# Kernel tuning notes

Measured on AMD Instinct MI355X. Metric: run time of the kernel, lower is better.

The kernel has to match this reference:

```python
import jax, jax.numpy as jnp
import numpy as np

D = 512
M_FUT = 3
EPS = 1e-12


def _lin(x, W, b):
    return x @ W + b


def _svd_orthogonalize(m):
    # m: [B, 9] -> [B, 3, 3] SO(3) via SVD orthogonalization (special Procrustes)
    m = m.reshape(-1, 3, 3)
    norm = jnp.maximum(jnp.linalg.norm(m, axis=-1, keepdims=True), EPS)
    mt = jnp.swapaxes(m / norm, -1, -2)          # normalize rows, then transpose
    u, s, vh = jnp.linalg.svd(mt, full_matrices=False)
    v = jnp.swapaxes(vh, -1, -2)                 # torch.svd returns V, jax returns V^H
    ut = jnp.swapaxes(u, -1, -2)
    det = jnp.linalg.det(jnp.matmul(v, ut))      # [B]
    v_adj = jnp.concatenate([v[:, :, :-1], v[:, :, -1:] * det[:, None, None]], axis=2)
    return jnp.matmul(v_adj, ut)


def setup_inputs() -> dict:
    key = jax.random.key(0)
    ks = iter(jax.random.split(key, 40))
    B, N, M = 32, 3, M_FUT
    ph = pw = 37
    BN, hw = B * N, ph * pw
    sc = 1.0 / np.sqrt(D)
    rn = lambda *shape: (jax.random.normal(next(ks), shape, dtype=jnp.float32) * sc)
    inp = {
        'feat': jax.random.normal(next(ks), (BN, hw, D), dtype=jnp.float32),
        'patch_h': ph, 'patch_w': pw, 'batch_size': B, 'num_current_frames': N,
        # two ResConvBlocks, three 512x512 Linears each (in==out -> skip is identity)
        'W_res': rn(2, 3, D, D), 'b_res': rn(2, 3, D),
        # TemporalCameraMLP
        'W_cur1': rn(D, D), 'b_cur1': rn(D), 'W_cur2': rn(D, D), 'b_cur2': rn(D),
        'W_tp1': rn(D, D), 'b_tp1': rn(D), 'W_tp2': rn(D, D * M), 'b_tp2': rn(D * M),
        'W_fut1': rn(D, D), 'b_fut1': rn(D), 'W_fut2': rn(D, D), 'b_fut2': rn(D),
        # more_mlps
        'W_m1': rn(D, D), 'b_m1': rn(D), 'W_m2': rn(D, D), 'b_m2': rn(D),
        # pose heads (fp32)
        'W_t': rn(D, 3), 'b_t': rn(3), 'W_r': rn(D, 9), 'b_r': rn(9),
    }
    return inp


def reference(feat, patch_h, patch_w, batch_size, num_current_frames,
              W_res, b_res, W_cur1, b_cur1, W_cur2, b_cur2,
              W_tp1, b_tp1, W_tp2, b_tp2, W_fut1, b_fut1, W_fut2, b_fut2,
              W_m1, b_m1, W_m2, b_m2, W_t, b_t, W_r, b_r):
    B, N = batch_size, num_current_frames
    M = W_tp2.shape[1] // W_tp2.shape[0]
    # stacked residual 1x1-conv (Linear) blocks
    for i in range(2):
        x = jax.nn.relu(_lin(feat, W_res[i, 0], b_res[i, 0]))
        x = jax.nn.relu(_lin(x, W_res[i, 1], b_res[i, 1]))
        x = jax.nn.relu(_lin(x, W_res[i, 2], b_res[i, 2]))
        feat = feat + x
    # AdaptiveAvgPool2d(1) over patch grid == mean over hw
    pooled = feat.mean(axis=1)                                  # [BN, D]
    # TemporalCameraMLP
    cur = _lin(jax.nn.relu(_lin(pooled, W_cur1, b_cur1)), W_cur2, b_cur2)   # [BN, D]
    gctx = pooled.reshape(B, N, -1).mean(axis=1)                            # [B, D]
    tf = _lin(jax.nn.relu(_lin(gctx, W_tp1, b_tp1)), W_tp2, b_tp2)          # [B, D*M]
    tf = tf.reshape(B * M, -1)
    fut = _lin(jax.nn.relu(_lin(tf, W_fut1, b_fut1)), W_fut2, b_fut2)       # [B*M, D]
    allf = jnp.concatenate([cur, fut], axis=0)                              # [B*(N+M), D]
    h = jax.nn.relu(_lin(jax.nn.relu(_lin(allf, W_m1, b_m1)), W_m2, b_m2))
    # pose head in fp32
    hf = h.astype(jnp.float32)
    out_t = _lin(hf, W_t, b_t)                                  # [newBN, 3]
    out_r = _lin(hf, W_r, b_r)                                  # [newBN, 9]
    r = _svd_orthogonalize(out_r)                               # [newBN, 3, 3]
    newBN = allf.shape[0]
    pose = jnp.zeros((newBN, 4, 4), dtype=jnp.float32)
    pose = pose.at[:, :3, :3].set(r)
    pose = pose.at[:, :3, 3].set(out_t)
    pose = pose.at[:, 3, 3].set(1.0)
    return pose
```

## Files before the change

### kernel.cpp

```cpp
#include <hip/hip_runtime.h>


typedef unsigned short u16;
typedef __attribute__((ext_vector_type(8))) short short8;
typedef __attribute__((ext_vector_type(16))) float f32x16;

constexpr int  DDIM   = 512;
constexpr long R_ROWS = 96L * 1369L;
constexpr long R_PAD  = 2054L * 64L;

__device__ __forceinline__ u16 f2b(float f) {
  union { float f; unsigned u; } x; x.f = f;
  unsigned r = (x.u + 0x7FFFu + ((x.u >> 16) & 1u)) >> 16;
  return (u16)r;
}
__device__ __forceinline__ float b2f(u16 b) {
  union { unsigned u; float f; } x; x.u = ((unsigned)b) << 16;
  return x.f;
}

__global__ void convert_feat_k(const float* __restrict__ in, u16* __restrict__ out) {
  long i4 = ((long)blockIdx.x * 256 + threadIdx.x) * 4;
  if (i4 >= R_PAD * DDIM) return;
  ushort4 o;
  if (i4 < R_ROWS * DDIM) {
    float4 v = *(const float4*)(in + i4);
    o.x = f2b(v.x); o.y = f2b(v.y); o.z = f2b(v.z); o.w = f2b(v.w);
  } else {
    o.x = 0; o.y = 0; o.z = 0; o.w = 0;
  }
  *(ushort4*)(out + i4) = o;
}

__global__ void pack_w_k(const float* __restrict__ W, u16* __restrict__ Wp) {
  int tid = blockIdx.x * 256 + threadIdx.x;
  if (tid >= 6 * 262144) return;
  int g  = tid >> 18, t2 = tid & 262143;
  int ks = t2 >> 13, t3 = t2 & 8191;
  int q  = t3 >> 12, t4 = t3 & 4095;
  int n  = t4 >> 3,  j  = t4 & 7;
  int k  = ks * 16 + q * 8 + j;
  Wp[tid] = f2b(W[(long)g * 262144 + (long)k * 512 + n]);
}

__global__ __launch_bounds__(256, 2)
void fused_res_k(u16* __restrict__ Xg, const u16* __restrict__ Wp,
                 const float* __restrict__ bres) {
  __shared__ u16 Yb[64 * 512];
  const int tid = threadIdx.x;
  const int lane = tid & 63;
  const int wvC  = tid >> 6;
  const int l31  = lane & 31;
  const int q    = lane >> 5;
  const long rowBase = (long)blockIdx.x * 64;

#pragma unroll
  for (int i = 0; i < 16; ++i) {
    int L = i * 256 + tid;
    int r = L >> 6, cS = L & 63;
    int c = cS ^ r;
    const u16* ga = Xg + (rowBase + r) * DDIM + c * 8;
    __builtin_amdgcn_global_load_lds(
        (const __attribute__((address_space(1))) void*)ga,
        (__attribute__((address_space(3))) void*)&Yb[L * 8], 16, 0, 0);
  }
  __syncthreads();

  for (int l = 0; l < 3; ++l) {
    const u16* wl = Wp + (long)l * 262144;
    const float* bias = bres + l * 512;

    f32x16 acc[4][2];
#pragma unroll
    for (int mi = 0; mi < 4; ++mi)
#pragma unroll
      for (int nb = 0; nb < 2; ++nb)
#pragma unroll
        for (int e = 0; e < 16; ++e) acc[mi][nb][e] = 0.f;

#pragma unroll 4
    for (int ks = 0; ks < 32; ++ks) {
      const int k8 = ks * 2 + q;
      const u16* wk = wl + ((long)(k8) * 512 + wvC * 128 + l31) * 8;
      short8 wf[4];
#pragma unroll
      for (int mi = 0; mi < 4; ++mi)
        wf[mi] = *(const short8*)(wk + mi * 32 * 8);
      short8 xf[2];
#pragma unroll
      for (int nb = 0; nb < 2; ++nb) {
        int r = nb * 32 + l31;
        xf[nb] = *(const short8*)&Yb[(r * 64 + (k8 ^ r)) * 8];
      }
#pragma unroll
      for (int mi = 0; mi < 4; ++mi)
#pragma unroll
        for (int nb = 0; nb < 2; ++nb)
          acc[mi][nb] = __builtin_amdgcn_mfma_f32_32x32x16_bf16(
              wf[mi], xf[nb], acc[mi][nb], 0, 0, 0);
    }
    __syncthreads();

    if (l < 2) {
#pragma unroll
      for (int mi = 0; mi < 4; ++mi) {
#pragma unroll
        for (int j2 = 0; j2 < 4; ++j2) {
          int n0 = wvC * 128 + mi * 32 + 4 * q + 8 * j2;
          float4 bv = *(const float4*)(bias + n0);
#pragma unroll
          for (int nb = 0; nb < 2; ++nb) {
            int r = nb * 32 + l31;
            ushort4 pk;
            pk.x = f2b(fmaxf(acc[mi][nb][4 * j2 + 0] + bv.x, 0.f));
            pk.y = f2b(fmaxf(acc[mi][nb][4 * j2 + 1] + bv.y, 0.f));
            pk.z = f2b(fmaxf(acc[mi][nb][4 * j2 + 2] + bv.z, 0.f));
            pk.w = f2b(fmaxf(acc[mi][nb][4 * j2 + 3] + bv.w, 0.f));
            *(ushort4*)&Yb[(r * 64 + ((n0 >> 3) ^ r)) * 8 + (n0 & 7)] = pk;
          }
        }
      }
      __syncthreads();
    } else {
#pragma unroll
      for (int mi = 0; mi < 4; ++mi) {
#pragma unroll
        for (int j2 = 0; j2 < 4; ++j2) {
          int n0 = wvC * 128 + mi * 32 + 4 * q + 8 * j2;
          float4 bv = *(const float4*)(bias + n0);
#pragma unroll
          for (int nb = 0; nb < 2; ++nb) {
            int r = nb * 32 + l31;
            u16* gp = Xg + (rowBase + r) * DDIM + n0;
            ushort4 xv = *(const ushort4*)gp;
            ushort4 pk;
            pk.x = f2b(fmaxf(acc[mi][nb][4 * j2 + 0] + bv.x, 0.f) + b2f(xv.x));
            pk.y = f2b(fmaxf(acc[mi][nb][4 * j2 + 1] + bv.y, 0.f) + b2f(xv.y));
            pk.z = f2b(fmaxf(acc[mi][nb][4 * j2 + 2] + bv.z, 0.f) + b2f(xv.z));
            pk.w = f2b(fmaxf(acc[mi][nb][4 * j2 + 3] + bv.w, 0.f) + b2f(xv.w));
            *(ushort4*)gp = pk;
          }
        }
      }
    }
  }
}

__global__ void zero_k(float* p, int n) {
  int i = blockIdx.x * 256 + threadIdx.x;
  if (i < n) p[i] = 0.f;
}

__global__ void pool_k(const u16* __restrict__ feat, float* __restrict__ pooled) {
  int bn = blockIdx.x, ch = blockIdx.y, d = threadIdx.x;
  int p0 = ch * 172, p1 = p0 + 172;
  if (p1 > 1369) p1 = 1369;
  float s = 0.f;
  long base = ((long)bn * 1369 + p0) * DDIM + d;
  for (int p = p0; p < p1; ++p) { s += b2f(feat[base]); base += DDIM; }
  atomicAdd(&pooled[bn * DDIM + d], s * (1.0f / 1369.0f));
}

__global__ void gctx_k(const float* __restrict__ pooled, float* __restrict__ gctx) {
  int i = blockIdx.x * 256 + threadIdx.x;
  if (i >= 32 * DDIM) return;
  int b = i >> 9, d = i & 511;
  const float* p = pooled + (long)b * 3 * DDIM + d;
  gctx[i] = (p[0] + p[DDIM] + p[2 * DDIM]) * (1.0f / 3.0f);
}

template <bool RELU>
__global__ void lin_k(const float* __restrict__ in, const float* __restrict__ W,
                      const float* __restrict__ bias, float* __restrict__ out,
                      int K, int N) {
  int n = blockIdx.x * 256 + threadIdx.x;
  int r = blockIdx.y;
  if (n >= N) return;
  float acc = bias[n];
  const float* xi = in + (long)r * K;
#pragma unroll 8
  for (int k = 0; k < K; ++k) acc = fmaf(xi[k], W[(long)k * N + n], acc);
  if (RELU) acc = fmaxf(acc, 0.f);
  out[(long)r * N + n] = acc;
}

__global__ void pose_k(const float* __restrict__ h,
                       const float* __restrict__ Wt, const float* __restrict__ bt,
                       const float* __restrict__ Wr, const float* __restrict__ br,
                       float* __restrict__ out) {
  int row = blockIdx.x;
  int lane = threadIdx.x;
  const float* hr = h + (long)row * DDIM;
  float part[12];
#pragma unroll
  for (int c = 0; c < 12; ++c) {
    float acc = 0.f;
    for (int k = lane; k < DDIM; k += 64) {
      float wvv = (c < 3) ? Wt[k * 3 + c] : Wr[k * 9 + (c - 3)];
      acc += hr[k] * wvv;
    }
#pragma unroll
    for (int off = 32; off > 0; off >>= 1) acc += __shfl_down(acc, off);
    part[c] = acc;
  }
  if (lane != 0) return;

  double t3[3];
  for (int i = 0; i < 3; ++i) t3[i] = (double)part[i] + (double)bt[i];
  double m[3][3];
  for (int i = 0; i < 3; ++i)
    for (int j = 0; j < 3; ++j) m[i][j] = (double)part[3 + i * 3 + j] + (double)br[i * 3 + j];
  for (int i = 0; i < 3; ++i) {
    double nn = sqrt(m[i][0] * m[i][0] + m[i][1] * m[i][1] + m[i][2] * m[i][2]);
    if (nn < 1e-12) nn = 1e-12;
    m[i][0] /= nn; m[i][1] /= nn; m[i][2] /= nn;
  }
  double Km[3][3];
  for (int a = 0; a < 3; ++a)
    for (int b = 0; b < 3; ++b) {
      double s = 0;
      for (int i = 0; i < 3; ++i) s += m[i][a] * m[i][b];
      Km[a][b] = s;
    }
  double V[3][3] = {{1, 0, 0}, {0, 1, 0}, {0, 0, 1}};
  const int PQ[3][2] = {{0, 1}, {0, 2}, {1, 2}};
  for (int sweep = 0; sweep < 20; ++sweep) {
    for (int e = 0; e < 3; ++e) {
      int p = PQ[e][0], qq = PQ[e][1];
      double apq = Km[p][qq];
      if (apq == 0.0) continue;
      double tau = (Km[qq][qq] - Km[p][p]) / (2.0 * apq);
      double tt = (tau >= 0.0 ? 1.0 : -1.0) / (fabs(tau) + sqrt(1.0 + tau * tau));
      double cc = 1.0 / sqrt(1.0 + tt * tt), ss = tt * cc;
      for (int k = 0; k < 3; ++k) { double a1 = Km[p][k], a2 = Km[qq][k]; Km[p][k] = cc * a1 - ss * a2; Km[qq][k] = ss * a1 + cc * a2; }
      for (int k = 0; k < 3; ++k) { double a1 = Km[k][p], a2 = Km[k][qq]; Km[k][p] = cc * a1 - ss * a2; Km[k][qq] = ss * a1 + cc * a2; }
      for (int k = 0; k < 3; ++k) { double a1 = V[k][p], a2 = V[k][qq]; V[k][p] = cc * a1 - ss * a2; V[k][qq] = ss * a1 + cc * a2; }
    }
  }
  double lam[3] = {Km[0][0], Km[1][1], Km[2][2]};
  int o0 = 0, o1 = 1, o2 = 2; double detV = 1.0;
  if (lam[o0] < lam[o1]) { int t = o0; o0 = o1; o1 = t; detV = -detV; }
  if (lam[o1] < lam[o2]) { int t = o1; o1 = o2; o2 = t; detV = -detV; }
  if (lam[o0] < lam[o1]) { int t = o0; o0 = o1; o1 = t; detV = -detV; }
  double v0[3] = {V[0][o0], V[1][o0], V[2][o0]};
  double v1[3] = {V[0][o1], V[1][o1], V[2][o1]};
  double v2[3] = {V[0][o2], V[1][o2], V[2][o2]};
  double u0[3], u1[3];
  for (int i = 0; i < 3; ++i) u0[i] = m[i][0] * v0[0] + m[i][1] * v0[1] + m[i][2] * v0[2];
  double n0 = sqrt(u0[0] * u0[0] + u0[1] * u0[1] + u0[2] * u0[2]); if (n0 < 1e-30) n0 = 1e-30;
  for (int i = 0; i < 3; ++i) u0[i] /= n0;
  for (int i = 0; i < 3; ++i) u1[i] = m[i][0] * v1[0] + m[i][1] * v1[1] + m[i][2] * v1[2];
  double d01 = u0[0] * u1[0] + u0[1] * u1[1] + u0[2] * u1[2];
  for (int i = 0; i < 3; ++i) u1[i] -= d01 * u0[i];
  double n1 = sqrt(u1[0] * u1[0] + u1[1] * u1[1] + u1[2] * u1[2]); if (n1 < 1e-30) n1 = 1e-30;
  for (int i = 0; i < 3; ++i) u1[i] /= n1;
  double u2[3] = {u0[1] * u1[2] - u0[2] * u1[1],
                  u0[2] * u1[0] - u0[0] * u1[2],
                  u0[0] * u1[1] - u0[1] * u1[0]};
  float* o = out + (long)row * 16;
  for (int i = 0; i < 3; ++i) {
    for (int j = 0; j < 3; ++j)
      o[i * 4 + j] = (float)(u0[i] * v0[j] + u1[i] * v1[j] + detV * u2[i] * v2[j]);
    o[i * 4 + 3] = (float)t3[i];
  }
  o[12] = 0.f; o[13] = 0.f; o[14] = 0.f; o[15] = 1.f;
}

extern "C" void kernel_launch(void* const* d_in, const int* in_sizes, int n_in,
                              void* d_out, int out_size, void* d_ws, size_t ws_size,
                              hipStream_t stream) {
  (void)in_sizes; (void)n_in; (void)out_size; (void)ws_size;
  const float* feat   = (const float*)d_in[0];
  const float* W_res  = (const float*)d_in[5];
  const float* b_res  = (const float*)d_in[6];
  const float* W_cur1 = (const float*)d_in[7];
  const float* b_cur1 = (const float*)d_in[8];
  const float* W_cur2 = (const float*)d_in[9];
  const float* b_cur2 = (const float*)d_in[10];
  const float* W_tp1  = (const float*)d_in[11];
  const float* b_tp1  = (const float*)d_in[12];
  const float* W_tp2  = (const float*)d_in[13];
  const float* b_tp2  = (const float*)d_in[14];
  const float* W_fut1 = (const float*)d_in[15];
  const float* b_fut1 = (const float*)d_in[16];
  const float* W_fut2 = (const float*)d_in[17];
  const float* b_fut2 = (const float*)d_in[18];
  const float* W_m1   = (const float*)d_in[19];
  const float* b_m1   = (const float*)d_in[20];
  const float* W_m2   = (const float*)d_in[21];
  const float* b_m2   = (const float*)d_in[22];
  const float* W_t    = (const float*)d_in[23];
  const float* b_t    = (const float*)d_in[24];
  const float* W_r    = (const float*)d_in[25];
  const float* b_r    = (const float*)d_in[26];

  char* ws = (char*)d_ws;
  const size_t SZ_BIG = (size_t)R_PAD * DDIM * 2;
  u16* A  = (u16*)(ws);
  u16* Wp = (u16*)(ws + SZ_BIG);
  char* tail = ws + SZ_BIG + (size_t)6 * 262144 * 2;
  float* pooled = (float*)(tail);
  float* gctx   = pooled + 96 * 512;
  float* tmp    = gctx + 32 * 512;
  float* tfb    = tmp + 192 * 512;
  float* allf   = tfb + 32 * 1536;
  float* h2     = allf + 192 * 512;
  float* outp   = (float*)d_out;

  convert_feat_k<<<65728, 256, 0, stream>>>(feat, A);
  pack_w_k<<<6144, 256, 0, stream>>>(W_res, Wp);

  fused_res_k<<<2054, 256, 0, stream>>>(A, Wp,                 b_res);
  fused_res_k<<<2054, 256, 0, stream>>>(A, Wp + 3L * 262144,   b_res + 3 * 512);

  zero_k<<<(96 * 512 + 255) / 256, 256, 0, stream>>>(pooled, 96 * 512);
  pool_k<<<dim3(96, 8), 512, 0, stream>>>(A, pooled);
  gctx_k<<<(32 * 512 + 255) / 256, 256, 0, stream>>>(pooled, gctx);

  lin_k<true ><<<dim3(2, 96),  256, 0, stream>>>(pooled, W_cur1, b_cur1, tmp, 512, 512);
  lin_k<false><<<dim3(2, 96),  256, 0, stream>>>(tmp, W_cur2, b_cur2, allf, 512, 512);
  lin_k<true ><<<dim3(2, 32),  256, 0, stream>>>(gctx, W_tp1, b_tp1, tmp, 512, 512);
  lin_k<false><<<dim3(6, 32),  256, 0, stream>>>(tmp, W_tp2, b_tp2, tfb, 512, 1536);
  lin_k<true ><<<dim3(2, 96),  256, 0, stream>>>(tfb, W_fut1, b_fut1, tmp, 512, 512);
  lin_k<false><<<dim3(2, 96),  256, 0, stream>>>(tmp, W_fut2, b_fut2, allf + 96 * 512, 512, 512);
  lin_k<true ><<<dim3(2, 192), 256, 0, stream>>>(allf, W_m1, b_m1, tmp, 512, 512);
  lin_k<true ><<<dim3(2, 192), 256, 0, stream>>>(tmp, W_m2, b_m2, h2, 512, 512);

  pose_k<<<192, 64, 0, stream>>>(h2, W_t, b_t, W_r, b_r, outp);
}
```

Baseline: 1.675 ms.

## Fuse feat conversion and both residual blocks into one trunk kernel, fuse MLP tail

Folds the fp32-to-bf16 conversion into a single trunk kernel that runs all six 512x512 layers of both residual blocks with activations kept in LDS. It uses 512 threads with 64 columns per wave and software-pipelined weight and LDS fragment loads. The nine small MLP and pose launches become one 24-block tail kernel that chains the layers through shared memory. This removes several global round-trips of the large activation tensor and many launch overheads, at the cost of a low-parallelism tail kernel and a different register/occupancy profile in the trunk.

```diff
diff --git a/kernel.cpp b/kernel.cpp
--- a/kernel.cpp
+++ b/kernel.cpp
@@ -19,129 +19,125 @@
   return x.f;
 }
 
-__global__ void convert_feat_k(const float* __restrict__ in, u16* __restrict__ out) {
-  long i4 = ((long)blockIdx.x * 256 + threadIdx.x) * 4;
-  if (i4 >= R_PAD * DDIM) return;
-  ushort4 o;
-  if (i4 < R_ROWS * DDIM) {
-    float4 v = *(const float4*)(in + i4);
-    o.x = f2b(v.x); o.y = f2b(v.y); o.z = f2b(v.z); o.w = f2b(v.w);
-  } else {
-    o.x = 0; o.y = 0; o.z = 0; o.w = 0;
-  }
-  *(ushort4*)(out + i4) = o;
-}
-
 __global__ void pack_w_k(const float* __restrict__ W, u16* __restrict__ Wp) {
   int tid = blockIdx.x * 256 + threadIdx.x;
   if (tid >= 6 * 262144) return;
   int g  = tid >> 18, t2 = tid & 262143;
-  int ks = t2 >> 13, t3 = t2 & 8191;
-  int q  = t3 >> 12, t4 = t3 & 4095;
-  int n  = t4 >> 3,  j  = t4 & 7;
-  int k  = ks * 16 + q * 8 + j;
+  int k8 = t2 >> 12, t3 = t2 & 4095;
+  int n  = t3 >> 3,  j  = t3 & 7;
+  int k  = k8 * 8 + j;
   Wp[tid] = f2b(W[(long)g * 262144 + (long)k * 512 + n]);
 }
 
-__global__ __launch_bounds__(256, 2)
-void fused_res_k(u16* __restrict__ Xg, const u16* __restrict__ Wp,
-                 const float* __restrict__ bres) {
+__global__ __launch_bounds__(512, 3)
+void trunk_k(const float* __restrict__ feat, u16* __restrict__ A,
+             const u16* __restrict__ Wp, const float* __restrict__ bres) {
   __shared__ u16 Yb[64 * 512];
-  const int tid = threadIdx.x;
+  const int tid  = threadIdx.x;
   const int lane = tid & 63;
-  const int wvC  = tid >> 6;
+  const int wv   = tid >> 6;
   const int l31  = lane & 31;
   const int q    = lane >> 5;
+  const int colBase = wv * 64;
   const long rowBase = (long)blockIdx.x * 64;
 
 #pragma unroll
   for (int i = 0; i < 16; ++i) {
-    int L = i * 256 + tid;
-    int r = L >> 6, cS = L & 63;
-    int c = cS ^ r;
-    const u16* ga = Xg + (rowBase + r) * DDIM + c * 8;
-    __builtin_amdgcn_global_load_lds(
-        (const __attribute__((address_space(1))) void*)ga,
-        (__attribute__((address_space(3))) void*)&Yb[L * 8], 16, 0, 0);
+    int f4 = i * 512 + tid;
+    int r = f4 >> 7, c4 = f4 & 127;
+    int k = c4 * 4;
+    long grow = rowBase + r;
+    float4 v = {0.f, 0.f, 0.f, 0.f};
+    if (grow < R_ROWS) v = *(const float4*)(feat + grow * DDIM + k);
+    ushort4 pk;
+    pk.x = f2b(v.x); pk.y = f2b(v.y); pk.z = f2b(v.z); pk.w = f2b(v.w);
+    int k8 = c4 >> 1, half = c4 & 1;
+    *(ushort4*)&Yb[(r * 64 + (k8 ^ r)) * 8 + half * 4] = pk;
+    *(ushort4*)(A + grow * DDIM + k) = pk;
   }
   __syncthreads();
 
-  for (int l = 0; l < 3; ++l) {
+  for (int l = 0; l < 6; ++l) {
     const u16* wl = Wp + (long)l * 262144;
     const float* bias = bres + l * 512;
 
-    f32x16 acc[4][2];
-#pragma unroll
-    for (int mi = 0; mi < 4; ++mi)
+    f32x16 acc[2][2];
+#pragma unroll
+    for (int mi = 0; mi < 2; ++mi)
 #pragma unroll
       for (int nb = 0; nb < 2; ++nb)
 #pragma unroll
         for (int e = 0; e < 16; ++e) acc[mi][nb][e] = 0.f;
 
-#pragma unroll 4
-    for (int ks = 0; ks < 32; ++ks) {
-      const int k8 = ks * 2 + q;
-      const u16* wk = wl + ((long)(k8) * 512 + wvC * 128 + l31) * 8;
-      short8 wf[4];
-#pragma unroll
-      for (int mi = 0; mi < 4; ++mi)
-        wf[mi] = *(const short8*)(wk + mi * 32 * 8);
-      short8 xf[2];
+    auto loadW = [&](short8* w, int ks) {
+      const u16* wk = wl + ((long)(ks * 2 + q) * 512 + colBase + l31) * 8;
+      w[0] = *(const short8*)wk;
+      w[1] = *(const short8*)(wk + 32 * 8);
+    };
+    auto loadX = [&](short8* x, int ks) {
+      int k8 = ks * 2 + q;
 #pragma unroll
       for (int nb = 0; nb < 2; ++nb) {
         int r = nb * 32 + l31;
-        xf[nb] = *(const short8*)&Yb[(r * 64 + (k8 ^ r)) * 8];
+        x[nb] = *(const short8*)&Yb[(r * 64 + (k8 ^ r)) * 8];
       }
-#pragma unroll
-      for (int mi = 0; mi < 4; ++mi)
+    };
+
+    short8 wA[2], wB[2], xA[2];
+    loadW(wA, 0); loadW(wB, 1); loadX(xA, 0);
+#pragma unroll
+    for (int ks = 0; ks < 32; ++ks) {
+      short8 wC[2], xN[2];
+      loadW(wC, ks < 30 ? ks + 2 : ks);
+      loadX(xN, ks < 31 ? ks + 1 : ks);
+#pragma unroll
+      for (int mi = 0; mi < 2; ++mi)
 #pragma unroll
         for (int nb = 0; nb < 2; ++nb)
           acc[mi][nb] = __builtin_amdgcn_mfma_f32_32x32x16_bf16(
-              wf[mi], xf[nb], acc[mi][nb], 0, 0, 0);
+              wA[mi], xA[nb], acc[mi][nb], 0, 0, 0);
+      wA[0] = wB[0]; wA[1] = wB[1];
+      wB[0] = wC[0]; wB[1] = wC[1];
+      xA[0] = xN[0]; xA[1] = xN[1];
     }
     __syncthreads();
 
-    if (l < 2) {
-#pragma unroll
-      for (int mi = 0; mi < 4; ++mi) {
-#pragma unroll
-        for (int j2 = 0; j2 < 4; ++j2) {
-          int n0 = wvC * 128 + mi * 32 + 4 * q + 8 * j2;
-          float4 bv = *(const float4*)(bias + n0);
-#pragma unroll
-          for (int nb = 0; nb < 2; ++nb) {
-            int r = nb * 32 + l31;
-            ushort4 pk;
-            pk.x = f2b(fmaxf(acc[mi][nb][4 * j2 + 0] + bv.x, 0.f));
-            pk.y = f2b(fmaxf(acc[mi][nb][4 * j2 + 1] + bv.y, 0.f));
-            pk.z = f2b(fmaxf(acc[mi][nb][4 * j2 + 2] + bv.z, 0.f));
-            pk.w = f2b(fmaxf(acc[mi][nb][4 * j2 + 3] + bv.w, 0.f));
-            *(ushort4*)&Yb[(r * 64 + ((n0 >> 3) ^ r)) * 8 + (n0 & 7)] = pk;
-          }
+#pragma unroll
+    for (int mi = 0; mi < 2; ++mi) {
+#pragma unroll
+      for (int j2 = 0; j2 < 4; ++j2) {
+        int n0 = colBase + mi * 32 + 4 * q + 8 * j2;
+        float4 bv = *(const float4*)(bias + n0);
+#pragma unroll
+        for (int nb = 0; nb < 2; ++nb) {
+          int r = nb * 32 + l31;
+          ushort4 pk;
+          pk.x = f2b(fmaxf(acc[mi][nb][4 * j2 + 0] + bv.x, 0.f));
+          pk.y = f2b(fmaxf(acc[mi][nb][4 * j2 + 1] + bv.y, 0.f));
+          pk.z = f2b(fmaxf(acc[mi][nb][4 * j2 + 2] + bv.z, 0.f));
+          pk.w = f2b(fmaxf(acc[mi][nb][4 * j2 + 3] + bv.w, 0.f));
+          *(ushort4*)&Yb[(r * 64 + ((n0 >> 3) ^ r)) * 8 + (n0 & 7)] = pk;
         }
       }
+    }
+    __syncthreads();
+
+    if (l == 2 || l == 5) {
+#pragma unroll
+      for (int i = 0; i < 8; ++i) {
+        int L = i * 512 + tid;
+        int r = L >> 6, cS = L & 63, c = cS ^ r;
+        long off = (rowBase + r) * DDIM + c * 8;
+        short8 y = *(const short8*)&Yb[L * 8];
+        short8 rs = *(const short8*)(A + off);
+        short8 o;
+#pragma unroll
+        for (int e = 0; e < 8; ++e)
+          o[e] = (short)f2b(b2f((u16)y[e]) + b2f((u16)rs[e]));
+        *(short8*)(A + off) = o;
+        if (l == 2) *(short8*)&Yb[L * 8] = o;
+      }
       __syncthreads();
-    } else {
-#pragma unroll
-      for (int mi = 0; mi < 4; ++mi) {
-#pragma unroll
-        for (int j2 = 0; j2 < 4; ++j2) {
-          int n0 = wvC * 128 + mi * 32 + 4 * q + 8 * j2;
-          float4 bv = *(const float4*)(bias + n0);
-#pragma unroll
-          for (int nb = 0; nb < 2; ++nb) {
-            int r = nb * 32 + l31;
-            u16* gp = Xg + (rowBase + r) * DDIM + n0;
-            ushort4 xv = *(const ushort4*)gp;
-            ushort4 pk;
-            pk.x = f2b(fmaxf(acc[mi][nb][4 * j2 + 0] + bv.x, 0.f) + b2f(xv.x));
-            pk.y = f2b(fmaxf(acc[mi][nb][4 * j2 + 1] + bv.y, 0.f) + b2f(xv.y));
-            pk.z = f2b(fmaxf(acc[mi][nb][4 * j2 + 2] + bv.z, 0.f) + b2f(xv.z));
-            pk.w = f2b(fmaxf(acc[mi][nb][4 * j2 + 3] + bv.w, 0.f) + b2f(xv.w));
-            *(ushort4*)gp = pk;
-          }
-        }
-      }
     }
   }
 }
@@ -151,65 +147,22 @@
   if (i < n) p[i] = 0.f;
 }
 
-__global__ void pool_k(const u16* __restrict__ feat, float* __restrict__ pooled) {
+__global__ void pool_k(const u16* __restrict__ A, float* __restrict__ pooled) {
   int bn = blockIdx.x, ch = blockIdx.y, d = threadIdx.x;
   int p0 = ch * 172, p1 = p0 + 172;
   if (p1 > 1369) p1 = 1369;
   float s = 0.f;
   long base = ((long)bn * 1369 + p0) * DDIM + d;
-  for (int p = p0; p < p1; ++p) { s += b2f(feat[base]); base += DDIM; }
+#pragma unroll 4
+  for (int p = p0; p < p1; ++p) { s += b2f(A[base]); base += DDIM; }
   atomicAdd(&pooled[bn * DDIM + d], s * (1.0f / 1369.0f));
 }
 
-__global__ void gctx_k(const float* __restrict__ pooled, float* __restrict__ gctx) {
-  int i = blockIdx.x * 256 + threadIdx.x;
-  if (i >= 32 * DDIM) return;
-  int b = i >> 9, d = i & 511;
-  const float* p = pooled + (long)b * 3 * DDIM + d;
-  gctx[i] = (p[0] + p[DDIM] + p[2 * DDIM]) * (1.0f / 3.0f);
-}
-
-template <bool RELU>
-__global__ void lin_k(const float* __restrict__ in, const float* __restrict__ W,
-                      const float* __restrict__ bias, float* __restrict__ out,
-                      int K, int N) {
-  int n = blockIdx.x * 256 + threadIdx.x;
-  int r = blockIdx.y;
-  if (n >= N) return;
-  float acc = bias[n];
-  const float* xi = in + (long)r * K;
-#pragma unroll 8
-  for (int k = 0; k < K; ++k) acc = fmaf(xi[k], W[(long)k * N + n], acc);
-  if (RELU) acc = fmaxf(acc, 0.f);
-  out[(long)r * N + n] = acc;
-}
-
-__global__ void pose_k(const float* __restrict__ h,
-                       const float* __restrict__ Wt, const float* __restrict__ bt,
-                       const float* __restrict__ Wr, const float* __restrict__ br,
-                       float* __restrict__ out) {
-  int row = blockIdx.x;
-  int lane = threadIdx.x;
-  const float* hr = h + (long)row * DDIM;
-  float part[12];
-#pragma unroll
-  for (int c = 0; c < 12; ++c) {
-    float acc = 0.f;
-    for (int k = lane; k < DDIM; k += 64) {
-      float wvv = (c < 3) ? Wt[k * 3 + c] : Wr[k * 9 + (c - 3)];
-      acc += hr[k] * wvv;
-    }
-#pragma unroll
-    for (int off = 32; off > 0; off >>= 1) acc += __shfl_down(acc, off);
-    part[c] = acc;
-  }
-  if (lane != 0) return;
-
-  double t3[3];
-  for (int i = 0; i < 3; ++i) t3[i] = (double)part[i] + (double)bt[i];
+__device__ void svd_pose(const float* pin, float* o) {
+  double t3[3] = {pin[0], pin[1], pin[2]};
   double m[3][3];
   for (int i = 0; i < 3; ++i)
-    for (int j = 0; j < 3; ++j) m[i][j] = (double)part[3 + i * 3 + j] + (double)br[i * 3 + j];
+    for (int j = 0; j < 3; ++j) m[i][j] = (double)pin[3 + i * 3 + j];
   for (int i = 0; i < 3; ++i) {
     double nn = sqrt(m[i][0] * m[i][0] + m[i][1] * m[i][1] + m[i][2] * m[i][2]);
     if (nn < 1e-12) nn = 1e-12;
@@ -257,13 +210,96 @@
   double u2[3] = {u0[1] * u1[2] - u0[2] * u1[1],
                   u0[2] * u1[0] - u0[0] * u1[2],
                   u0[0] * u1[1] - u0[1] * u1[0]};
-  float* o = out + (long)row * 16;
   for (int i = 0; i < 3; ++i) {
     for (int j = 0; j < 3; ++j)
       o[i * 4 + j] = (float)(u0[i] * v0[j] + u1[i] * v1[j] + detV * u2[i] * v2[j]);
     o[i * 4 + 3] = (float)t3[i];
   }
   o[12] = 0.f; o[13] = 0.f; o[14] = 0.f; o[15] = 1.f;
+}
+
+__global__ void tail_k(const float* __restrict__ pooled,
+                       const float* Wc1, const float* bc1, const float* Wc2, const float* bc2,
+                       const float* Wt1, const float* bt1, const float* Wt2, const float* bt2,
+                       const float* Wf1, const float* bf1, const float* Wf2, const float* bf2,
+                       const float* Wm1, const float* bm1, const float* Wm2, const float* bm2,
+                       const float* Wt, const float* bt, const float* Wr, const float* br,
+                       float* __restrict__ out) {
+  __shared__ float bufA[8][512];
+  __shared__ float bufB[8][512];
+  __shared__ float pose_in[8][12];
+  const int blk = blockIdx.x;
+  const int tid = threadIdx.x;
+  const bool isFut = blk >= 12;
+  int m0 = 0, b0 = 0;
+  if (!isFut) {
+    int r0 = blk * 8;
+#pragma unroll
+    for (int r = 0; r < 8; ++r) bufA[r][tid] = pooled[(r0 + r) * 512 + tid];
+  } else {
+    int f = blk - 12; m0 = f >> 2; b0 = (f & 3) * 8;
+#pragma unroll
+    for (int r = 0; r < 8; ++r) {
+      int b = b0 + r;
+      bufA[r][tid] = (pooled[(b * 3 + 0) * 512 + tid] +
+                      pooled[(b * 3 + 1) * 512 + tid] +
+                      pooled[(b * 3 + 2) * 512 + tid]) * (1.0f / 3.0f);
+    }
+  }
+  __syncthreads();
+
+  auto layer = [&](float (*in)[512], float (*ob)[512], const float* W, int ldw,
+                   int coff, const float* b, bool relu) {
+    int n = tid;
+    float acc[8];
+#pragma unroll
+    for (int r = 0; r < 8; ++r) acc[r] = b[coff + n];
+    for (int k = 0; k < 512; k += 4) {
+      float w0 = W[(long)(k + 0) * ldw + coff + n];
+      float w1 = W[(long)(k + 1) * ldw + coff + n];
+      float w2 = W[(long)(k + 2) * ldw + coff + n];
+      float w3 = W[(long)(k + 3) * ldw + coff + n];
+#pragma unroll
+      for (int r = 0; r < 8; ++r) {
+        float4 x = *(const float4*)&in[r][k];
+        acc[r] = fmaf(x.x, w0, acc[r]);
+        acc[r] = fmaf(x.y, w1, acc[r]);
+        acc[r] = fmaf(x.z, w2, acc[r]);
+        acc[r] = fmaf(x.w, w3, acc[r]);
+      }
+    }
+#pragma unroll
+    for (int r = 0; r < 8; ++r) ob[r][n] = relu ? fmaxf(acc[r], 0.f) : acc[r];
+    __syncthreads();
+  };
+
+  if (!isFut) {
+    layer(bufA, bufB, Wc1, 512, 0, bc1, true);
+    layer(bufB, bufA, Wc2, 512, 0, bc2, false);
+    layer(bufA, bufB, Wm1, 512, 0, bm1, true);
+    layer(bufB, bufA, Wm2, 512, 0, bm2, true);
+  } else {
+    layer(bufA, bufB, Wt1, 512, 0, bt1, true);
+    layer(bufB, bufA, Wt2, 1536, m0 * 512, bt2, false);
+    layer(bufA, bufB, Wf1, 512, 0, bf1, true);
+    layer(bufB, bufA, Wf2, 512, 0, bf2, false);
+    layer(bufA, bufB, Wm1, 512, 0, bm1, true);
+    layer(bufB, bufA, Wm2, 512, 0, bm2, true);
+  }
+  int r = tid >> 6, c = tid & 63;
+  if (c < 12) {
+    float acc = (c < 3) ? bt[c] : br[c - 3];
+    for (int k = 0; k < 512; ++k) {
+      float w = (c < 3) ? Wt[k * 3 + c] : Wr[k * 9 + (c - 3)];
+      acc = fmaf(bufA[r][k], w, acc);
+    }
+    pose_in[r][c] = acc;
+  }
+  __syncthreads();
+  if (tid < 8) {
+    int grow = isFut ? (96 + (b0 + tid) * 3 + m0) : (blk * 8 + tid);
+    svd_pose(&pose_in[tid][0], out + (long)grow * 16);
+  }
 }
 
 extern "C" void kernel_launch(void* const* d_in, const int* in_sizes, int n_in,
@@ -298,33 +334,17 @@
   const size_t SZ_BIG = (size_t)R_PAD * DDIM * 2;
   u16* A  = (u16*)(ws);
   u16* Wp = (u16*)(ws + SZ_BIG);
-  char* tail = ws + SZ_BIG + (size_t)6 * 262144 * 2;
-  float* pooled = (float*)(tail);
-  float* gctx   = pooled + 96 * 512;
-  float* tmp    = gctx + 32 * 512;
-  float* tfb    = tmp + 192 * 512;
-  float* allf   = tfb + 32 * 1536;
-  float* h2     = allf + 192 * 512;
+  float* pooled = (float*)(ws + SZ_BIG + (size_t)6 * 262144 * 2);
   float* outp   = (float*)d_out;
 
-  convert_feat_k<<<65728, 256, 0, stream>>>(feat, A);
   pack_w_k<<<6144, 256, 0, stream>>>(W_res, Wp);
-
-  fused_res_k<<<2054, 256, 0, stream>>>(A, Wp,                 b_res);
-  fused_res_k<<<2054, 256, 0, stream>>>(A, Wp + 3L * 262144,   b_res + 3 * 512);
+  trunk_k<<<2054, 512, 0, stream>>>(feat, A, Wp, b_res);
 
   zero_k<<<(96 * 512 + 255) / 256, 256, 0, stream>>>(pooled, 96 * 512);
   pool_k<<<dim3(96, 8), 512, 0, stream>>>(A, pooled);
-  gctx_k<<<(32 * 512 + 255) / 256, 256, 0, stream>>>(pooled, gctx);
-
-  lin_k<true ><<<dim3(2, 96),  256, 0, stream>>>(pooled, W_cur1, b_cur1, tmp, 512, 512);
-  lin_k<false><<<dim3(2, 96),  256, 0, stream>>>(tmp, W_cur2, b_cur2, allf, 512, 512);
-  lin_k<true ><<<dim3(2, 32),  256, 0, stream>>>(gctx, W_tp1, b_tp1, tmp, 512, 512);
-  lin_k<false><<<dim3(6, 32),  256, 0, stream>>>(tmp, W_tp2, b_tp2, tfb, 512, 1536);
-  lin_k<true ><<<dim3(2, 96),  256, 0, stream>>>(tfb, W_fut1, b_fut1, tmp, 512, 512);
-  lin_k<false><<<dim3(2, 96),  256, 0, stream>>>(tmp, W_fut2, b_fut2, allf + 96 * 512, 512, 512);
-  lin_k<true ><<<dim3(2, 192), 256, 0, stream>>>(allf, W_m1, b_m1, tmp, 512, 512);
-  lin_k<true ><<<dim3(2, 192), 256, 0, stream>>>(tmp, W_m2, b_m2, h2, 512, 512);
-
-  pose_k<<<192, 64, 0, stream>>>(h2, W_t, b_t, W_r, b_r, outp);
-}
+
+  tail_k<<<24, 512, 0, stream>>>(pooled,
+      W_cur1, b_cur1, W_cur2, b_cur2, W_tp1, b_tp1, W_tp2, b_tp2,
+      W_fut1, b_fut1, W_fut2, b_fut2, W_m1, b_m1, W_m2, b_m2,
+      W_t, b_t, W_r, b_r, outp);
+}
```

New measurement: 1.984 ms. 1.18x slower.
